# Kernel tuning notes

Measured on AMD Instinct MI355X. Metric: run time of the kernel, lower is better.

The kernel has to match this reference:

```python
import jax, jax.numpy as jnp
import numpy as np

K = 3        # kernel_size
STRIDE = 1
PAD = 1
DIL = 1


def setup_inputs() -> dict:
    key = jax.random.key(0)
    ks = jax.random.split(key, 5)
    B, C, H, W, O = 4, 64, 128, 128, 64
    x = jax.random.normal(ks[0], (B, C, H, W), jnp.float32)
    # small offset-conv weights -> offsets of a few pixels (realistic trained regime)
    offset_w = jax.random.normal(ks[1], (2 * K * K, C, K, K), jnp.float32) * 0.01
    offset_b = jax.random.normal(ks[2], (2 * K * K,), jnp.float32) * 0.01
    weight = jax.random.normal(ks[3], (O, C, K, K), jnp.float32)
    bias = jax.random.normal(ks[4], (O,), jnp.float32)
    return {"x": x, "offset_w": offset_w, "offset_b": offset_b,
            "weight": weight, "bias": bias}


def _conv2d(x, w, b):
    y = jax.lax.conv_general_dilated(
        x, w, window_strides=(STRIDE, STRIDE),
        padding=[(PAD, PAD), (PAD, PAD)],
        dimension_numbers=("NCHW", "OIHW", "NCHW"))
    return y + b[None, :, None, None]


def _deform_conv2d(x, offset, weight, bias):
    B, C, H, W = x.shape
    O = weight.shape[0]
    KK = K * K
    Ho, Wo = offset.shape[2], offset.shape[3]
    # offset channels ordered (y, x) per kernel tap: [B, KK, 2, Ho, Wo]
    off = offset.reshape(B, KK, 2, Ho, Wo)
    kyy, kxx = jnp.meshgrid(jnp.arange(K) * DIL, jnp.arange(K) * DIL, indexing="ij")
    kyy = kyy.reshape(KK).astype(x.dtype)
    kxx = kxx.reshape(KK).astype(x.dtype)
    base_y = (jnp.arange(Ho) * STRIDE - PAD).astype(x.dtype)
    base_x = (jnp.arange(Wo) * STRIDE - PAD).astype(x.dtype)
    # sampling positions [B, KK, Ho, Wo]
    py = base_y[None, None, :, None] + kyy[None, :, None, None] + off[:, :, 0]
    px = base_x[None, None, None, :] + kxx[None, :, None, None] + off[:, :, 1]

    y0 = jnp.floor(py); x0 = jnp.floor(px)
    y1 = y0 + 1.0;      x1 = x0 + 1.0
    wy1 = py - y0; wy0 = 1.0 - wy1
    wx1 = px - x0; wx0 = 1.0 - wx1

    xf = x.reshape(B, C, H * W)

    def corner(yc, xc):
        valid = (yc >= 0) & (yc < H) & (xc >= 0) & (xc < W)  # zero padding outside
        idx = (jnp.clip(yc, 0, H - 1) * W + jnp.clip(xc, 0, W - 1)).astype(jnp.int32)
        g = jax.vmap(lambda xb, ib: xb[:, ib.reshape(-1)])(xf, idx)  # [B, C, KK*Ho*Wo]
        g = g.reshape(B, C, KK, Ho, Wo)
        return g * valid[:, None].astype(x.dtype)

    val = (corner(y0, x0) * (wy0 * wx0)[:, None]
         + corner(y0, x1) * (wy0 * wx1)[:, None]
         + corner(y1, x0) * (wy1 * wx0)[:, None]
         + corner(y1, x1) * (wy1 * wx1)[:, None])  # [B, C, KK, Ho, Wo]

    out = jnp.einsum("bckhw,ock->bohw", val, weight.reshape(O, C, KK))
    return out + bias[None, :, None, None]


def reference(x, offset_w, offset_b, weight, bias):
    offset = _conv2d(x, offset_w, offset_b)
    return _deform_conv2d(x, offset, weight, bias)
```

## Files before the change

kernel.cpp:

```cpp
#include <hip/hip_runtime.h>

#define B_   4
#define C_   64
#define O_   64
#define H_   128
#define W_   128
#define HW_  (H_ * W_)
#define KK_  9
#define M_   18

typedef short  short8  __attribute__((ext_vector_type(8)));
typedef float  floatx4 __attribute__((ext_vector_type(4)));
typedef float  float2v __attribute__((ext_vector_type(2)));
typedef unsigned int   uint4v   __attribute__((ext_vector_type(4)));
typedef unsigned short ushort8v __attribute__((ext_vector_type(8)));

static __device__ __forceinline__ unsigned short f2bf(float f) {
    unsigned int u = __float_as_uint(f);
    u += 0x7FFFu + ((u >> 16) & 1u);
    return (unsigned short)(u >> 16);
}
static __device__ __forceinline__ float2v bf2x(unsigned int q) {
    float2v r;
    r.x = __uint_as_float(q << 16);
    r.y = __uint_as_float(q & 0xFFFF0000u);
    return r;
}
static __device__ __forceinline__ float2v pk_mul(float2v a, float2v b) {
    float2v d;
    asm("v_pk_mul_f32 %0, %1, %2" : "=v"(d) : "v"(a), "v"(b));
    return d;
}
static __device__ __forceinline__ float2v pk_fma(float2v a, float2v b, float2v c) {
    float2v d;
    asm("v_pk_fma_f32 %0, %1, %2, %3" : "=v"(d) : "v"(a), "v"(b), "v"(c));
    return d;
}

__global__ __launch_bounds__(256) void prep(
        const float* __restrict__ x, const float* __restrict__ w,
        const float* __restrict__ ow, unsigned short* __restrict__ xT,
        unsigned short* __restrict__ wtbf, unsigned short* __restrict__ owtbf) {
    const int blk = blockIdx.x;
    if (blk < 1024) {
        __shared__ unsigned short T[64][70];
        const int tid  = threadIdx.x;
        const int half = blk & 1;
        const int y    = (blk >> 1) & (H_ - 1);
        const int b    = blk >> 8;
        const float* xby = x + (size_t)b * C_ * HW_ + y * W_ + half * 64;
        for (int i = tid; i < 64 * 64; i += 256) {
            const int c = i >> 6, xc = i & 63;
            T[xc][c] = f2bf(xby[(size_t)c * HW_ + xc]);
        }
        __syncthreads();
        for (int j = tid; j < 512; j += 256) {
            const int x8 = j >> 3, c8 = j & 7;
            const int gq  = c8 >> 1;
            const int sub = (c8 & 1) * 8;
            uint4v pk;
            #pragma unroll
            for (int k = 0; k < 4; ++k)
                pk[k] = *(const unsigned int*)&T[x8][c8 * 8 + k * 2];
            unsigned short* dst = xT
                + ((size_t)(b * 4 + gq) * HW_ + y * W_ + half * 64 + x8) * 16
                + sub;
            *(uint4v*)dst = pk;
        }
    } else if (blk < 1042) {
        const int i = (blk - 1024) * 256 + threadIdx.x;
        const int lane = i & 63, rest = i >> 6;
        const int ot = rest & 3, cks = rest >> 2;
        const int chunk = cks / 6, ks = cks % 6;
        const int o = ot * 16 + (lane & 15);
        const int kbase = chunk * 192 + ks * 32 + (lane >> 4) * 8;
        ushort8v pk;
        #pragma unroll
        for (int j = 0; j < 8; ++j) {
            const int k = kbase + j;
            pk[j] = f2bf(w[o * 576 + (k & 63) * 9 + (k >> 6)]);
        }
        *(ushort8v*)&wtbf[(size_t)i * 8] = pk;
    } else {
        const int i = (blk - 1042) * 256 + threadIdx.x;
        const int lane = i & 63, rest = i >> 6;
        const int tile = rest & 1, tks = rest >> 1;
        const int tap = tks >> 1, ks = tks & 1;
        const int m = tile * 16 + (lane & 15);
        const int cb = ks * 32 + (lane >> 4) * 8;
        ushort8v pk;
        #pragma unroll
        for (int j = 0; j < 8; ++j)
            pk[j] = (m < M_) ? f2bf(ow[m * 576 + (cb + j) * 9 + tap])
                             : (unsigned short)0;
        *(ushort8v*)&owtbf[(size_t)i * 8] = pk;
    }
}

__global__ __launch_bounds__(512, 6) void dcn_fused(
        const unsigned short* __restrict__ xT,
        const unsigned short* __restrict__ owtbf, const float* __restrict__ ob,
        const unsigned short* __restrict__ wtbf, const float* __restrict__ bias,
        float* __restrict__ out) {
    __shared__ unsigned short tile[5][68][64];
    __shared__ union {
        float offs[4][M_][16];
        float mrg[2][4][16][17];
    } v;

    const int tid    = threadIdx.x;
    const int lane   = tid & 63;
    const int wsl    = __builtin_amdgcn_readfirstlane(tid >> 6);
    const int p      = wsl & 3;
    const int h      = wsl >> 2;
    const int lane15 = lane & 15;
    const int quad   = lane >> 4;

    const int g    = blockIdx.x;
    const int xcd  = g & 7;
    const int slot = g >> 3;
    const int ho   = xcd * 16 + (slot >> 3);
    const int b    = (slot >> 1) & 3;
    const int wo_base = (slot & 1) << 6;

    const unsigned short* xTb = xT + (size_t)b * (4 * HW_ * 16);
    unsigned short* tp = &tile[0][0][0];

    for (int j = tid; j < 5 * 68 * 8; j += 512) {
        const int row = j / (68 * 8);
        const int rem = j - row * (68 * 8);
        const int px = rem >> 3, c8 = rem & 7;
        const int y  = ho - 2 + row;
        const int cx = wo_base - 2 + px;
        ushort8v p0 = {0, 0, 0, 0, 0, 0, 0, 0};
        if ((unsigned)y < (unsigned)H_ && (unsigned)cx < (unsigned)W_) {
            const int gq = c8 >> 1, sub = (c8 & 1) * 8;
            p0 = *(const ushort8v*)&xTb[(size_t)gq * (HW_ * 16)
                                        + ((size_t)y * W_ + cx) * 16 + sub];
        }
        const int sl = c8 ^ (px & 7);
        *(ushort8v*)&tp[(row * 68 + px) * 64 + sl * 8] = p0;
    }
    __syncthreads();

    {
        floatx4 oa = (floatx4){0.f, 0.f, 0.f, 0.f};
        #pragma unroll
        for (int ky = 0; ky < 3; ++ky) {
            #pragma unroll
            for (int kx = 0; kx < 3; ++kx) {
                const int tap = ky * 3 + kx;
                #pragma unroll
                for (int ks = 0; ks < 2; ++ks) {
                    const int pxA = p * 16 + lane15 + kx + 1;
                    const int sA  = (ks * 4 + quad) ^ (pxA & 7);
                    const short8 af = *(const short8*)
                        &tp[((ky + 1) * 68 + pxA) * 64 + sA * 8];
                    const int fb = ((tap * 2 + ks) * 2 + h) * 64 + lane;
                    const short8 bf = *(const short8*)&owtbf[(size_t)fb * 8];
                    oa = __builtin_amdgcn_mfma_f32_16x16x32_bf16(af, bf, oa, 0, 0, 0);
                }
            }
        }
        if (h == 0) {
            const float ob0 = ob[lane15];
            #pragma unroll
            for (int r = 0; r < 4; ++r) oa[r] += ob0;
            *(floatx4*)&v.offs[p][lane15][quad * 4] = oa;
        } else if (lane15 < 2) {
            const float ob1 = ob[16 + lane15];
            #pragma unroll
            for (int r = 0; r < 4; ++r) oa[r] += ob1;
            *(floatx4*)&v.offs[p][16 + lane15][quad * 4] = oa;
        }
    }
    __syncthreads();

    const int pxg = p * 16 + lane15;
    floatx4 acc[4];
    #pragma unroll
    for (int t = 0; t < 4; ++t) acc[t] = (floatx4){0.f, 0.f, 0.f, 0.f};

    #pragma unroll 2
    for (int k = h; k < 9; k += 2) {
        const int ky = k / 3, kx = k - ky * 3;
        const float offy = v.offs[p][2 * k][lane15];
        const float offx = v.offs[p][2 * k + 1][lane15];
        const float py  = (float)(ho - 1 + ky) + offy;
        const float pxx = (float)(wo_base - 1 + kx + pxg) + offx;
        const float fy = floorf(py), fx = floorf(pxx);
        const int y0 = (int)fy, x0 = (int)fx;
        const int y1 = y0 + 1,  x1 = x0 + 1;
        const float wy1 = py - fy,  wy0 = 1.f - wy1;
        const float wx1 = pxx - fx, wx0 = 1.f - wx1;
        const bool y0v = (unsigned)y0 < (unsigned)H_;
        const bool y1v = (unsigned)y1 < (unsigned)H_;
        const bool x0v = (unsigned)x0 < (unsigned)W_;
        const bool x1v = (unsigned)x1 < (unsigned)W_;
        const float w00 = (y0v && x0v) ? wy0 * wx0 : 0.f;
        const float w01 = (y0v && x1v) ? wy0 * wx1 : 0.f;
        const float w10 = (y1v && x0v) ? wy1 * wx0 : 0.f;
        const float w11 = (y1v && x1v) ? wy1 * wx1 : 0.f;
        const float2v w00_2 = {w00, w00};
        const float2v w01_2 = {w01, w01};
        const float2v w10_2 = {w10, w10};
        const float2v w11_2 = {w11, w11};
        const int ry0 = min(max(y0, 0), H_ - 1);
        const int ry1 = min(max(y1, 0), H_ - 1);
        const int cx0 = min(max(x0, 0), W_ - 1);
        const int cx1 = min(max(x1, 0), W_ - 1);
        const bool ok = (ry0 >= ho - 2) && (ry1 <= ho + 2) &&
                        (cx0 >= wo_base - 2) && (cx1 <= wo_base + 65);
        #pragma unroll
        for (int chalf = 0; chalf < 2; ++chalf) {
            const int c8 = chalf * 4 + quad;
            uint4v q00, q01, q10, q11;
            if (__all(ok)) {
                const int r0 = (ry0 - (ho - 2)) * 68;
                const int r1 = (ry1 - (ho - 2)) * 68;
                const int p0 = cx0 - (wo_base - 2);
                const int p1 = cx1 - (wo_base - 2);
                q00 = *(const uint4v*)&tp[(r0 + p0) * 64 + ((c8 ^ (p0 & 7)) * 8)];
                q01 = *(const uint4v*)&tp[(r0 + p1) * 64 + ((c8 ^ (p1 & 7)) * 8)];
                q10 = *(const uint4v*)&tp[(r1 + p0) * 64 + ((c8 ^ (p0 & 7)) * 8)];
                q11 = *(const uint4v*)&tp[(r1 + p1) * 64 + ((c8 ^ (p1 & 7)) * 8)];
            } else {
                const int c0 = chalf * 32 + quad * 8;
                const unsigned short* xp =
                    xTb + (size_t)(c0 >> 4) * (HW_ * 16) + (c0 & 8);
                q00 = *(const uint4v*)&xp[(ry0 * W_ + cx0) * 16];
                q01 = *(const uint4v*)&xp[(ry0 * W_ + cx1) * 16];
                q10 = *(const uint4v*)&xp[(ry1 * W_ + cx0) * 16];
                q11 = *(const uint4v*)&xp[(ry1 * W_ + cx1) * 16];
            }
            uint4v pw;
            #pragma unroll
            for (int j = 0; j < 4; ++j) {
                float2v vv = pk_mul(bf2x(q00[j]), w00_2);
                vv = pk_fma(bf2x(q01[j]), w01_2, vv);
                vv = pk_fma(bf2x(q10[j]), w10_2, vv);
                vv = pk_fma(bf2x(q11[j]), w11_2, vv);
                pw[j] = __builtin_amdgcn_perm(
                    __float_as_uint(vv.y) + 0x8000u,
                    __float_as_uint(vv.x) + 0x8000u,
                    0x07060302u);
            }
            const short8 af = *(const short8*)&pw;
            const int cks = k * 2 + chalf;
            const unsigned short* wb = wtbf + (size_t)cks * 2048 + lane * 8;
            #pragma unroll
            for (int t = 0; t < 4; ++t) {
                const short8 bfrag = *(const short8*)&wb[(size_t)t * 512];
                acc[t] = __builtin_amdgcn_mfma_f32_16x16x32_bf16(
                             af, bfrag, acc[t], 0, 0, 0);
            }
        }
    }
    __syncthreads();

    #pragma unroll
    for (int ph = 0; ph < 2; ++ph) {
        if (h == 1) {
            #pragma unroll
            for (int tt = 0; tt < 2; ++tt)
                #pragma unroll
                for (int r = 0; r < 4; ++r)
                    v.mrg[tt][p][lane15][quad * 4 + r] = acc[ph * 2 + tt][r];
        }
        __syncthreads();
        if (h == 0) {
            #pragma unroll
            for (int tt = 0; tt < 2; ++tt) {
                const float bs = bias[(ph * 2 + tt) * 16 + lane15];
                #pragma unroll
                for (int r = 0; r < 4; ++r)
                    v.mrg[tt][p][lane15][quad * 4 + r] +=
                        acc[ph * 2 + tt][r] + bs;
            }
        }
        __syncthreads();
        {
            const int t2   = tid >> 8;
            const int o16  = (tid >> 4) & 15;
            const int px64 = (tid & 15) * 4;
            const int pp   = px64 >> 4, wi = px64 & 15;
            floatx4 val;
            #pragma unroll
            for (int kq = 0; kq < 4; ++kq)
                val[kq] = v.mrg[t2][pp][o16][wi + kq];
            const int o = (ph * 2 + t2) * 16 + o16;
            *(floatx4*)&out[(size_t)(b * O_ + o) * HW_ + ho * W_ + wo_base + px64]
                = val;
        }
        __syncthreads();
    }
}

extern "C" void kernel_launch(void* const* d_in, const int* in_sizes, int n_in,
                              void* d_out, int out_size, void* d_ws, size_t ws_size,
                              hipStream_t stream) {
    const float* x    = (const float*)d_in[0];
    const float* ow   = (const float*)d_in[1];
    const float* ob   = (const float*)d_in[2];
    const float* w    = (const float*)d_in[3];
    const float* bias = (const float*)d_in[4];
    float* out = (float*)d_out;

    unsigned short* wtbf  = (unsigned short*)d_ws;
    unsigned short* owtbf = wtbf + 4608 * 8;
    unsigned short* xT    = owtbf + 2304 * 8;

    prep<<<1051, 256, 0, stream>>>(x, w, ow, xT, wtbf, owtbf);
    dcn_fused<<<B_ * H_ * (W_ / 64), 512, 0, stream>>>(xT, owtbf, ob, wtbf, bias, out);
}
```

Before: 111.0 us.

## Fuse x transpose and bf16 conversion into main kernel tile load

Removes the separate pass that converted x to a channel-interleaved bf16 layout in global memory. The main kernel now reads fp32 x directly in NCHW, converts channel pairs to bf16, and writes them into the swizzled shared-memory tile. The out-of-tile fallback path also gathers fp32 values from eight channel planes and converts them on the fly. This saves writing and re-reading a roughly 8 MB intermediate and shrinks the prep kernel. In exchange, tile loads become 4-byte strided accesses instead of 16-byte vector loads, and x halo rows are re-read and re-converted by neighbouring blocks.

Measured after the change: 130.0 us. +17.1%, slower.

```diff
diff --git a/kernel.cpp b/kernel.cpp
--- a/kernel.cpp
+++ b/kernel.cpp
@@ -37,38 +37,12 @@
     return d;
 }
 
-__global__ __launch_bounds__(256) void prep(
-        const float* __restrict__ x, const float* __restrict__ w,
-        const float* __restrict__ ow, unsigned short* __restrict__ xT,
+__global__ __launch_bounds__(256) void prep_w(
+        const float* __restrict__ w, const float* __restrict__ ow,
         unsigned short* __restrict__ wtbf, unsigned short* __restrict__ owtbf) {
     const int blk = blockIdx.x;
-    if (blk < 1024) {
-        __shared__ unsigned short T[64][70];
-        const int tid  = threadIdx.x;
-        const int half = blk & 1;
-        const int y    = (blk >> 1) & (H_ - 1);
-        const int b    = blk >> 8;
-        const float* xby = x + (size_t)b * C_ * HW_ + y * W_ + half * 64;
-        for (int i = tid; i < 64 * 64; i += 256) {
-            const int c = i >> 6, xc = i & 63;
-            T[xc][c] = f2bf(xby[(size_t)c * HW_ + xc]);
-        }
-        __syncthreads();
-        for (int j = tid; j < 512; j += 256) {
-            const int x8 = j >> 3, c8 = j & 7;
-            const int gq  = c8 >> 1;
-            const int sub = (c8 & 1) * 8;
-            uint4v pk;
-            #pragma unroll
-            for (int k = 0; k < 4; ++k)
-                pk[k] = *(const unsigned int*)&T[x8][c8 * 8 + k * 2];
-            unsigned short* dst = xT
-                + ((size_t)(b * 4 + gq) * HW_ + y * W_ + half * 64 + x8) * 16
-                + sub;
-            *(uint4v*)dst = pk;
-        }
-    } else if (blk < 1042) {
-        const int i = (blk - 1024) * 256 + threadIdx.x;
+    if (blk < 18) {
+        const int i = blk * 256 + threadIdx.x;
         const int lane = i & 63, rest = i >> 6;
         const int ot = rest & 3, cks = rest >> 2;
         const int chunk = cks / 6, ks = cks % 6;
@@ -82,7 +56,7 @@
         }
         *(ushort8v*)&wtbf[(size_t)i * 8] = pk;
     } else {
-        const int i = (blk - 1042) * 256 + threadIdx.x;
+        const int i = (blk - 18) * 256 + threadIdx.x;
         const int lane = i & 63, rest = i >> 6;
         const int tile = rest & 1, tks = rest >> 1;
         const int tap = tks >> 1, ks = tks & 1;
@@ -98,7 +72,7 @@
 }
 
 __global__ __launch_bounds__(512, 6) void dcn_fused(
-        const unsigned short* __restrict__ xT,
+        const float* __restrict__ x,
         const unsigned short* __restrict__ owtbf, const float* __restrict__ ob,
         const unsigned short* __restrict__ wtbf, const float* __restrict__ bias,
         float* __restrict__ out) {
@@ -123,23 +97,26 @@
     const int b    = (slot >> 1) & 3;
     const int wo_base = (slot & 1) << 6;
 
-    const unsigned short* xTb = xT + (size_t)b * (4 * HW_ * 16);
+    const float* xb = x + (size_t)b * C_ * HW_;
     unsigned short* tp = &tile[0][0][0];
 
-    for (int j = tid; j < 5 * 68 * 8; j += 512) {
-        const int row = j / (68 * 8);
-        const int rem = j - row * (68 * 8);
-        const int px = rem >> 3, c8 = rem & 7;
-        const int y  = ho - 2 + row;
-        const int cx = wo_base - 2 + px;
-        ushort8v p0 = {0, 0, 0, 0, 0, 0, 0, 0};
+    for (int j = tid; j < 5 * 32 * 68; j += 512) {
+        const int row = j / (32 * 68);
+        const int rem = j - row * (32 * 68);
+        const int cp  = rem / 68;
+        const int px  = rem - cp * 68;
+        const int y   = ho - 2 + row;
+        const int cx  = wo_base - 2 + px;
+        unsigned int word = 0;
         if ((unsigned)y < (unsigned)H_ && (unsigned)cx < (unsigned)W_) {
-            const int gq = c8 >> 1, sub = (c8 & 1) * 8;
-            p0 = *(const ushort8v*)&xTb[(size_t)gq * (HW_ * 16)
-                                        + ((size_t)y * W_ + cx) * 16 + sub];
-        }
+            const int o = y * W_ + cx;
+            const float f0 = xb[(size_t)(2 * cp) * HW_ + o];
+            const float f1 = xb[(size_t)(2 * cp + 1) * HW_ + o];
+            word = (unsigned)f2bf(f0) | ((unsigned)f2bf(f1) << 16);
+        }
+        const int c8 = cp >> 2, ci = cp & 3;
         const int sl = c8 ^ (px & 7);
-        *(ushort8v*)&tp[(row * 68 + px) * 64 + sl * 8] = p0;
+        *(unsigned int*)&tp[(row * 68 + px) * 64 + sl * 8 + ci * 2] = word;
     }
     __syncthreads();
 
@@ -225,13 +202,18 @@
                 q10 = *(const uint4v*)&tp[(r1 + p0) * 64 + ((c8 ^ (p0 & 7)) * 8)];
                 q11 = *(const uint4v*)&tp[(r1 + p1) * 64 + ((c8 ^ (p1 & 7)) * 8)];
             } else {
-                const int c0 = chalf * 32 + quad * 8;
-                const unsigned short* xp =
-                    xTb + (size_t)(c0 >> 4) * (HW_ * 16) + (c0 & 8);
-                q00 = *(const uint4v*)&xp[(ry0 * W_ + cx0) * 16];
-                q01 = *(const uint4v*)&xp[(ry0 * W_ + cx1) * 16];
-                q10 = *(const uint4v*)&xp[(ry1 * W_ + cx0) * 16];
-                q11 = *(const uint4v*)&xp[(ry1 * W_ + cx1) * 16];
+                const float* xc = xb + (size_t)(chalf * 32 + quad * 8) * HW_;
+                const int o00 = ry0 * W_ + cx0, o01 = ry0 * W_ + cx1;
+                const int o10 = ry1 * W_ + cx0, o11 = ry1 * W_ + cx1;
+                #pragma unroll
+                for (int j2 = 0; j2 < 4; ++j2) {
+                    const float* xa = xc + (size_t)(2 * j2) * HW_;
+                    const float* xbp = xc + (size_t)(2 * j2 + 1) * HW_;
+                    q00[j2] = (unsigned)f2bf(xa[o00]) | ((unsigned)f2bf(xbp[o00]) << 16);
+                    q01[j2] = (unsigned)f2bf(xa[o01]) | ((unsigned)f2bf(xbp[o01]) << 16);
+                    q10[j2] = (unsigned)f2bf(xa[o10]) | ((unsigned)f2bf(xbp[o10]) << 16);
+                    q11[j2] = (unsigned)f2bf(xa[o11]) | ((unsigned)f2bf(xbp[o11]) << 16);
+                }
             }
             uint4v pw;
             #pragma unroll
@@ -308,8 +290,7 @@
 
     unsigned short* wtbf  = (unsigned short*)d_ws;
     unsigned short* owtbf = wtbf + 4608 * 8;
-    unsigned short* xT    = owtbf + 2304 * 8;
-
-    prep<<<1051, 256, 0, stream>>>(x, w, ow, xT, wtbf, owtbf);
-    dcn_fused<<<B_ * H_ * (W_ / 64), 512, 0, stream>>>(xT, owtbf, ob, wtbf, bias, out);
-}
+
+    prep_w<<<27, 256, 0, stream>>>(w, ow, wtbf, owtbf);
+    dcn_fused<<<B_ * H_ * (W_ / 64), 512, 0, stream>>>(x, owtbf, ob, wtbf, bias, out);
+}
```
